# Kernel tuning notes

Measured on AMD Instinct MI355X. Metric: run time of the kernel, lower is better.

## Reference

```python
import jax, jax.numpy as jnp
import numpy as np

N_HEADS = 32
N_KV = 16
HEAD_DIM = 128
REPEATS = N_HEADS // N_KV
ROPE_THETA = 10000.0
SOFTCAP = 50.0
SCALE = 1.0 / np.sqrt(144.0)


def _rope_cos_sin(L, dtype):
    half = HEAD_DIM // 2
    inv_freq = 1.0 / (ROPE_THETA ** (jnp.arange(0, HEAD_DIM, 2, dtype=jnp.float32) / HEAD_DIM))
    ang = jnp.arange(L, dtype=jnp.float32)[:, None] * inv_freq[None, :]  # [L, half]
    return jnp.cos(ang).astype(dtype), jnp.sin(ang).astype(dtype)


def _apply_rope(t, cos, sin):
    # t: [B, H, L, D]; non-traditional (rotate-half) RoPE
    half = HEAD_DIM // 2
    t1, t2 = t[..., :half], t[..., half:]
    c = cos[None, None, :, :]
    s = sin[None, None, :, :]
    return jnp.concatenate([t1 * c - t2 * s, t2 * c + t1 * s], axis=-1)


def setup_inputs() -> dict:
    key = jax.random.key(0)
    k1, k2, k3, k4, k5 = jax.random.split(key, 5)
    B, L, D = 1, 2048, 4608
    x = jax.random.normal(k1, (B, L, D), dtype=jnp.float32)
    wq = jax.random.normal(k2, (N_HEADS * HEAD_DIM, D), dtype=jnp.float32) * 0.02
    wk = jax.random.normal(k3, (N_KV * HEAD_DIM, D), dtype=jnp.float32) * 0.02
    wv = jax.random.normal(k4, (N_KV * HEAD_DIM, D), dtype=jnp.float32) * 0.02
    wo = jax.random.normal(k5, (D, N_HEADS * HEAD_DIM), dtype=jnp.float32) * 0.02
    mask = jnp.tril(jnp.ones((L, L), dtype=bool))  # causal
    return {"x": x, "mask": mask, "wq": wq, "wk": wk, "wv": wv, "wo": wo}


def reference(x, mask, wq, wk, wv, wo):
    B, L, D = x.shape
    q = (x @ wq.T).reshape(B, L, N_HEADS, HEAD_DIM).transpose(0, 2, 1, 3)
    k = (x @ wk.T).reshape(B, L, N_KV, HEAD_DIM).transpose(0, 2, 1, 3)
    v = (x @ wv.T).reshape(B, L, N_KV, HEAD_DIM).transpose(0, 2, 1, 3)

    cos, sin = _rope_cos_sin(L, x.dtype)
    q = _apply_rope(q, cos, sin) * jnp.asarray(SCALE, x.dtype)
    k = _apply_rope(k, cos, sin)

    # GQA: group queries per kv head -> [B, n_kv, repeats, L, D]
    qg = q.reshape(B, N_KV, REPEATS, L, HEAD_DIM)
    scores = jnp.einsum("bgrqd,bgkd->bgrqk", qg, k)
    scores = jnp.tanh(scores / SOFTCAP) * SOFTCAP
    neg = jnp.asarray(jnp.finfo(scores.dtype).min, scores.dtype)
    scores = jnp.where(mask[None, None, None, :, :], scores, neg)
    probs = jax.nn.softmax(scores, axis=-1)
    out = jnp.einsum("bgrqk,bgkd->bgrqd", probs, v)  # [B, n_kv, rep, L, D]
    out = out.reshape(B, N_HEADS, L, HEAD_DIM).transpose(0, 2, 1, 3).reshape(B, L, -1)
    return out @ wo.T
```

## Files before the change

### kernel.cpp

```cpp
#include <hip/hip_runtime.h>
#include <hip/hip_bf16.h>
#include <math.h>

typedef unsigned short u16;
typedef __attribute__((ext_vector_type(8))) short s16x8;
typedef __attribute__((ext_vector_type(4))) float f32x4;

#define SCALE 0.083333333333333329f
#define LDO 4128

__device__ __forceinline__ u16 f2bf(float f) {
    unsigned u = __float_as_uint(f);
    unsigned r = 0x7fffu + ((u >> 16) & 1u);
    return (u16)((u + r) >> 16);
}
__device__ __forceinline__ float bf2f(u16 v) {
    return __uint_as_float(((unsigned)v) << 16);
}

__global__ __launch_bounds__(256) void cast_kernel(const float* __restrict__ in,
                                                   u16* __restrict__ out) {
    size_t i = ((size_t)blockIdx.x * 256 + threadIdx.x) * 4;
    float4 v = *(const float4*)(in + i);
    ushort4 o;
    o.x = f2bf(v.x); o.y = f2bf(v.y); o.z = f2bf(v.z); o.w = f2bf(v.w);
    *(ushort4*)(out + i) = o;
}

__global__ __launch_bounds__(256) void cast_pad_kernel(const float* __restrict__ in,
                                                       u16* __restrict__ out) {
    size_t i = ((size_t)blockIdx.x * 256 + threadIdx.x) * 4;
    size_t row = i >> 12;
    int col = (int)(i & 4095);
    float4 v = *(const float4*)(in + i);
    ushort4 o;
    o.x = f2bf(v.x); o.y = f2bf(v.y); o.z = f2bf(v.z); o.w = f2bf(v.w);
    *(ushort4*)(out + row * LDO + col) = o;
}

__global__ __launch_bounds__(256) void rope_table_kernel(float* __restrict__ cosT,
                                                         float* __restrict__ sinT) {
    int idx = blockIdx.x * 256 + threadIdx.x;
    int i = idx & 63, pos = idx >> 6;
    float inv = __expf(-((float)i / 64.0f) * 9.210340371976184f);
    float ang = (float)pos * inv;
    cosT[idx] = cosf(ang);
    sinT[idx] = sinf(ang);
}

__global__ __launch_bounds__(256) void rope_q_kernel(const u16* __restrict__ T16,
                                                     u16* __restrict__ Qb,
                                                     const float* __restrict__ cosT,
                                                     const float* __restrict__ sinT) {
    int idx = blockIdx.x * 256 + threadIdx.x;
    int i = idx & 63;
    int head = (idx >> 6) & 31;
    int pos = idx >> 11;
    size_t rbase = (size_t)pos * 8192 + head * 128 + i;
    float t1 = bf2f(T16[rbase]), t2 = bf2f(T16[rbase + 64]);
    float c = cosT[(pos << 6) + i], s = sinT[(pos << 6) + i];
    size_t wbase = (size_t)pos * 4096 + head * 128 + i;
    Qb[wbase]      = f2bf((t1 * c - t2 * s) * SCALE);
    Qb[wbase + 64] = f2bf((t2 * c + t1 * s) * SCALE);
}

__global__ __launch_bounds__(256) void rope_k_kernel(const u16* __restrict__ T16,
                                                     u16* __restrict__ Kb,
                                                     const float* __restrict__ cosT,
                                                     const float* __restrict__ sinT) {
    int idx = blockIdx.x * 256 + threadIdx.x;
    int i = idx & 63;
    int head = (idx >> 6) & 15;
    int pos = idx >> 10;
    size_t rbase = (size_t)pos * 8192 + 4096 + head * 128 + i;
    float t1 = bf2f(T16[rbase]), t2 = bf2f(T16[rbase + 64]);
    float c = cosT[(pos << 6) + i], s = sinT[(pos << 6) + i];
    size_t wbase = (size_t)pos * 2048 + head * 128 + i;
    Kb[wbase]      = f2bf(t1 * c - t2 * s);
    Kb[wbase + 64] = f2bf(t2 * c + t1 * s);
}

__global__ __launch_bounds__(256) void vtrans_kernel(const u16* __restrict__ T16,
                                                     u16* __restrict__ Vt) {
    __shared__ u16 tile[32][33];
    int bc = (blockIdx.x & 63) << 5;
    int bl = (blockIdx.x >> 6) << 5;
    int x = threadIdx.x & 31, y = threadIdx.x >> 5;
    #pragma unroll
    for (int yy = y; yy < 32; yy += 8)
        tile[yy][x] = T16[(size_t)(bl + yy) * 8192 + 6144 + bc + x];
    __syncthreads();
    #pragma unroll
    for (int yy = y; yy < 32; yy += 8)
        Vt[(size_t)(bc + yy) * 2048 + bl + x] = tile[x][yy];
}

#define STAGE_A(buf, ktt, l)                                                            \
    __builtin_amdgcn_global_load_lds(                                                   \
        (const __attribute__((address_space(1))) unsigned int*)(aSrc + (size_t)(ktt) * 64 + (size_t)(l) * 64 * lda), \
        (__attribute__((address_space(3))) unsigned int*)(&lds[buf][0][(l) * 4096 + ldsoff]), 16, 0, 0)
#define STAGE_B(buf, ktt, l)                                                            \
    __builtin_amdgcn_global_load_lds(                                                   \
        (const __attribute__((address_space(1))) unsigned int*)(bSrc + (size_t)(ktt) * 64 + (size_t)(l) * 64 * ldb), \
        (__attribute__((address_space(3))) unsigned int*)(&lds[buf][1][(l) * 4096 + ldsoff]), 16, 0, 0)

template<bool OUT_BF16>
__device__ __forceinline__ void gemm256_core(const u16* __restrict__ A,
                                             const u16* __restrict__ B,
                                             void* __restrict__ C,
                                             int N, int K, int lda, int ldb,
                                             int bm, int bn,
                                             u16 (&lds)[2][2][16384]) {
    int t = threadIdx.x;
    int lane = t & 63, wave = t >> 6;
    int wm = wave >> 2, wn = wave & 3;
    int fr = lane & 15, fq = lane >> 4;
    int sw = (fr & 7) << 4;

    int srow = wave * 8 + (lane >> 3);
    int scb = ((lane & 7) * 16) ^ (((lane >> 3) & 7) << 4);
    const u16* aSrc = A + (size_t)(bm * 256 + srow) * lda + (scb >> 1);
    const u16* bSrc = B + (size_t)(bn * 256 + srow) * ldb + (scb >> 1);
    int ldsoff = wave * 512;

    f32x4 acc[8][4];
    #pragma unroll
    for (int m = 0; m < 8; m++)
        #pragma unroll
        for (int n = 0; n < 4; n++)
            acc[m][n] = (f32x4){0.f, 0.f, 0.f, 0.f};

    STAGE_B(0, 0, 0); STAGE_B(0, 0, 1); STAGE_B(0, 0, 2); STAGE_B(0, 0, 3);
    STAGE_A(0, 0, 0); STAGE_A(0, 0, 1); STAGE_A(0, 0, 2); STAGE_A(0, 0, 3);

    int nt = K >> 6;
    for (int it = 0; it < nt; ++it) {
        int cur = it & 1, nxt = cur ^ 1;
        bool more = (it + 1 < nt);
        const char* Ab = (const char*)&lds[cur][0][0];
        const char* Bb = (const char*)&lds[cur][1][0];
        int cb0 = (fq * 16) ^ sw;
        int cb1 = (64 + fq * 16) ^ sw;

        if (more) {
            STAGE_B(nxt, it + 1, 0); STAGE_B(nxt, it + 1, 1);
            __builtin_amdgcn_sched_barrier(0);
            asm volatile("s_waitcnt vmcnt(2)" ::: "memory");
        } else {
            asm volatile("s_waitcnt vmcnt(0)" ::: "memory");
        }
        __builtin_amdgcn_s_barrier();
        s16x8 b0[4], a0[4];
        #pragma unroll
        for (int n = 0; n < 4; ++n)
            b0[n] = *(const s16x8*)(Bb + (wn * 64 + n * 16 + fr) * 128 + cb0);
        #pragma unroll
        for (int m = 0; m < 4; ++m)
            a0[m] = *(const s16x8*)(Ab + (wm * 128 + m * 16 + fr) * 128 + cb0);
        __builtin_amdgcn_s_setprio(1);
        #pragma unroll
        for (int m = 0; m < 4; ++m)
            #pragma unroll
            for (int n = 0; n < 4; ++n)
                acc[m][n] = __builtin_amdgcn_mfma_f32_16x16x32_bf16(a0[m], b0[n], acc[m][n], 0, 0, 0);
        __builtin_amdgcn_s_setprio(0);
        s16x8 a1[4];
        #pragma unroll
        for (int m = 0; m < 4; ++m)
            a1[m] = *(const s16x8*)(Ab + (wm * 128 + (4 + m) * 16 + fr) * 128 + cb0);
        __builtin_amdgcn_s_barrier();

        if (more) { STAGE_B(nxt, it + 1, 2); STAGE_B(nxt, it + 1, 3); }
        __builtin_amdgcn_s_setprio(1);
        #pragma unroll
        for (int m = 0; m < 4; ++m)
            #pragma unroll
            for (int n = 0; n < 4; ++n)
                acc[4 + m][n] = __builtin_amdgcn_mfma_f32_16x16x32_bf16(a1[m], b0[n], acc[4 + m][n], 0, 0, 0);
        __builtin_amdgcn_s_setprio(0);
        s16x8 b1[4], a2[4];
        #pragma unroll
        for (int n = 0; n < 4; ++n)
            b1[n] = *(const s16x8*)(Bb + (wn * 64 + n * 16 + fr) * 128 + cb1);
        #pragma unroll
        for (int m = 0; m < 4; ++m)
            a2[m] = *(const s16x8*)(Ab + (wm * 128 + m * 16 + fr) * 128 + cb1);
        __builtin_amdgcn_s_barrier();

        if (more) {
            STAGE_A(nxt, it + 1, 0); STAGE_A(nxt, it + 1, 1);
            STAGE_A(nxt, it + 1, 2); STAGE_A(nxt, it + 1, 3);
        }
        __builtin_amdgcn_s_setprio(1);
        #pragma unroll
        for (int m = 0; m < 4; ++m)
            #pragma unroll
            for (int n = 0; n < 4; ++n)
                acc[m][n] = __builtin_amdgcn_mfma_f32_16x16x32_bf16(a2[m], b1[n], acc[m][n], 0, 0, 0);
        __builtin_amdgcn_s_setprio(0);
        s16x8 a3[4];
        #pragma unroll
        for (int m = 0; m < 4; ++m)
            a3[m] = *(const s16x8*)(Ab + (wm * 128 + (4 + m) * 16 + fr) * 128 + cb1);
        __builtin_amdgcn_s_barrier();

        __builtin_amdgcn_s_setprio(1);
        #pragma unroll
        for (int m = 0; m < 4; ++m)
            #pragma unroll
            for (int n = 0; n < 4; ++n)
                acc[4 + m][n] = __builtin_amdgcn_mfma_f32_16x16x32_bf16(a3[m], b1[n], acc[4 + m][n], 0, 0, 0);
        __builtin_amdgcn_s_setprio(0);
        __builtin_amdgcn_s_barrier();
    }

    #pragma unroll
    for (int m = 0; m < 8; ++m) {
        int row = bm * 256 + wm * 128 + m * 16 + fq * 4;
        #pragma unroll
        for (int n = 0; n < 4; ++n) {
            int col = bn * 256 + wn * 64 + n * 16 + fr;
            #pragma unroll
            for (int r = 0; r < 4; ++r) {
                if (OUT_BF16) ((u16*)C)[(size_t)(row + r) * N + col] = f2bf(acc[m][n][r]);
                else          ((float*)C)[(size_t)(row + r) * N + col] = acc[m][n][r];
            }
        }
    }
}

__global__ __launch_bounds__(512) void gemm256_qkv(const u16* __restrict__ A,
                                                   const u16* __restrict__ B,
                                                   u16* __restrict__ C, int K) {
    __shared__ u16 lds[2][2][16384];
    int bid = blockIdx.x;
    int x = bid & 7, j = bid >> 3;
    int bn = x * 4 + (j & 3);
    int bm = j >> 2;
    gemm256_core<true>(A, B, C, 8192, K, K, K, bm, bn, lds);
}

__global__ __launch_bounds__(512) void gemm256_out(const u16* __restrict__ A,
                                                   const u16* __restrict__ B,
                                                   float* __restrict__ C, int K) {
    __shared__ u16 lds[2][2][16384];
    int bid = blockIdx.x;
    int j = (bid & 7) * 18 + (bid >> 3);
    int bm = j & 7;
    int bn = j >> 3;
    gemm256_core<false>(A, B, C, 4608, K, LDO, LDO, bm, bn, lds);
}

__global__ __launch_bounds__(256) void attn_kernel(const u16* __restrict__ Qb,
                                                   const u16* __restrict__ Kb,
                                                   const u16* __restrict__ Vt,
                                                   u16* __restrict__ Ob) {
    __shared__ u16 Ks[64 * 128];
    __shared__ u16 Vs[128 * 64];
    __shared__ u16 Pst[4 * 1024];

    int bid = blockIdx.x;
    int hq = bid & 31;
    int qb = 31 - (bid >> 5);
    int g = hq >> 1;
    int t = threadIdx.x;
    int lane = t & 63, wave = t >> 6;
    int fr = lane & 15, fq = lane >> 4;
    int sw = (fr & 7) << 4;
    int qrow0 = qb * 64 + wave * 16;
    u16* Pw = &Pst[wave * 1024];

    s16x8 qf[4];
    #pragma unroll
    for (int s = 0; s < 4; s++)
        qf[s] = *(const s16x8*)&Qb[(size_t)(qrow0 + fr) * 4096 + hq * 128 + s * 32 + fq * 8];

    f32x4 o[8];
    #pragma unroll
    for (int c = 0; c < 8; c++) o[c] = (f32x4){0.f, 0.f, 0.f, 0.f};
    float liacc[4] = {0.f, 0.f, 0.f, 0.f};

    int w4 = wave * 4;
    int nT = qb + 1;
    for (int kt = 0; kt < nT; kt++) {
        int kv0 = kt << 6;
        __syncthreads();
        #pragma unroll
        for (int i = 0; i < 4; i++) {
            int li_ = w4 + i;
            int rk = li_ * 4 + (lane >> 4);
            int cbk = ((lane & 15) * 16) ^ ((rk & 7) << 4);
            const u16* srcK = Kb + (size_t)(kv0 + rk) * 2048 + g * 128 + (cbk >> 1);
            __builtin_amdgcn_global_load_lds(
                (const __attribute__((address_space(1))) unsigned int*)srcK,
                (__attribute__((address_space(3))) unsigned int*)(Ks + li_ * 512), 16, 0, 0);
            int rv = li_ * 8 + (lane >> 3);
            int cbv = ((lane & 7) * 16) ^ ((rv & 7) << 4);
            const u16* srcV = Vt + (size_t)(g * 128 + rv) * 2048 + kv0 + (cbv >> 1);
            __builtin_amdgcn_global_load_lds(
                (const __attribute__((address_space(1))) unsigned int*)srcV,
                (__attribute__((address_space(3))) unsigned int*)(Vs + li_ * 512), 16, 0, 0);
        }
        __syncthreads();

        if (kv0 <= qrow0 + 15) {
            f32x4 sf[4];
            #pragma unroll
            for (int j = 0; j < 4; j++) sf[j] = (f32x4){0.f, 0.f, 0.f, 0.f};
            #pragma unroll
            for (int j = 0; j < 4; j++)
                #pragma unroll
                for (int s = 0; s < 4; s++) {
                    s16x8 kf = *(const s16x8*)&Ks[(j * 16 + fr) * 128 + (((s * 64 + fq * 16) ^ sw) >> 1)];
                    sf[j] = __builtin_amdgcn_mfma_f32_16x16x32_bf16(qf[s], kf, sf[j], 0, 0, 0);
                }
            #pragma unroll
            for (int j = 0; j < 4; j++)
                #pragma unroll
                for (int r = 0; r < 4; r++) {
                    float s_ = sf[j][r];
                    float e = __builtin_amdgcn_exp2f(s_ * 0.05770780163f);
                    float p = __builtin_amdgcn_exp2f(-144.2695041f * __builtin_amdgcn_rcpf(e + 1.0f));
                    int colk = kv0 + j * 16 + fr;
                    int rowq = qrow0 + fq * 4 + r;
                    p = (colk > rowq) ? 0.0f : p;
                    sf[j][r] = p;
                    liacc[r] += p;
                }
            #pragma unroll
            for (int j = 0; j < 4; j++)
                #pragma unroll
                for (int r = 0; r < 4; r++) {
                    int row = fq * 4 + r, col = j * 16 + fr;
                    int byteoff = (row * 128 + col * 2) ^ ((row & 7) << 4);
                    *(u16*)((char*)Pw + byteoff) = f2bf(sf[j][r]);
                }
            #pragma unroll
            for (int s = 0; s < 2; s++) {
                int rbyte = (fr * 128 + s * 64 + fq * 16) ^ sw;
                s16x8 pf = *(const s16x8*)((const char*)Pw + rbyte);
                #pragma unroll
                for (int c = 0; c < 8; c++) {
                    s16x8 vf = *(const s16x8*)&Vs[(c * 16 + fr) * 64 + (((s * 64 + fq * 16) ^ sw) >> 1)];
                    o[c] = __builtin_amdgcn_mfma_f32_16x16x32_bf16(pf, vf, o[c], 0, 0, 0);
                }
            }
        }
    }
    #pragma unroll
    for (int d = 1; d < 16; d <<= 1)
        #pragma unroll
        for (int r = 0; r < 4; r++)
            liacc[r] += __shfl_xor(liacc[r], d);
    float rli[4];
    #pragma unroll
    for (int r = 0; r < 4; r++) rli[r] = __builtin_amdgcn_rcpf(liacc[r]);
    #pragma unroll
    for (int c = 0; c < 8; c++)
        #pragma unroll
        for (int r = 0; r < 4; r++) {
            int rowq = qrow0 + fq * 4 + r;
            Ob[(size_t)rowq * LDO + hq * 128 + c * 16 + fr] = f2bf(o[c][r] * rli[r]);
        }
}

extern "C" void kernel_launch(void* const* d_in, const int* in_sizes, int n_in,
                              void* d_out, int out_size, void* d_ws, size_t ws_size,
                              hipStream_t stream) {
    const float* x  = (const float*)d_in[0];
    const float* wq = (const float*)d_in[2];
    const float* wk = (const float*)d_in[3];
    const float* wv = (const float*)d_in[4];
    const float* wo = (const float*)d_in[5];
    float* out = (float*)d_out;

    char* w = (char*)d_ws;
    u16*   xb   = (u16*)(w);
    u16*   wb   = (u16*)(w + 18874368);
    u16*   T16  = (u16*)(w + 94371840);
    u16*   Ob   = (u16*)(w + 127926272);
    u16*   Qbuf = (u16*)(w + 144834560);
    u16*   Kbuf = (u16*)(w + 161611776);
    u16*   Vt   = (u16*)(w + 170000384);
    float* cosT = (float*)(w + 178388992);
    float* sinT = (float*)(w + 178913280);

    rope_table_kernel<<<512, 256, 0, stream>>>(cosT, sinT);
    cast_kernel<<<9216, 256, 0, stream>>>(x, xb);

    cast_kernel<<<18432, 256, 0, stream>>>(wq, wb);
    cast_kernel<<<9216, 256, 0, stream>>>(wk, wb + (size_t)4096 * 4608);
    cast_kernel<<<9216, 256, 0, stream>>>(wv, wb + (size_t)6144 * 4608);

    gemm256_qkv<<<256, 512, 0, stream>>>(xb, wb, T16, 4608);

    rope_q_kernel<<<16384, 256, 0, stream>>>(T16, Qbuf, cosT, sinT);
    rope_k_kernel<<<8192, 256, 0, stream>>>(T16, Kbuf, cosT, sinT);
    vtrans_kernel<<<4096, 256, 0, stream>>>(T16, Vt);

    attn_kernel<<<1024, 256, 0, stream>>>(Qbuf, Kbuf, Vt, Ob);

    cast_pad_kernel<<<18432, 256, 0, stream>>>(wo, wb);
    gemm256_out<<<144, 512, 0, stream>>>(Ob, wb, out, 4096);
}
```

Measured before the change: 398.7 us.

## Fuse fp32-to-bf16 weight conversion into GEMM B-tile staging

```diff
diff --git a/kernel.cpp b/kernel.cpp
--- a/kernel.cpp
+++ b/kernel.cpp
@@ -4,6 +4,7 @@
 
 typedef unsigned short u16;
 typedef __attribute__((ext_vector_type(8))) short s16x8;
+typedef __attribute__((ext_vector_type(8))) unsigned short u16x8;
 typedef __attribute__((ext_vector_type(4))) float f32x4;
 
 #define SCALE 0.083333333333333329f
@@ -25,17 +26,6 @@
     ushort4 o;
     o.x = f2bf(v.x); o.y = f2bf(v.y); o.z = f2bf(v.z); o.w = f2bf(v.w);
     *(ushort4*)(out + i) = o;
-}
-
-__global__ __launch_bounds__(256) void cast_pad_kernel(const float* __restrict__ in,
-                                                       u16* __restrict__ out) {
-    size_t i = ((size_t)blockIdx.x * 256 + threadIdx.x) * 4;
-    size_t row = i >> 12;
-    int col = (int)(i & 4095);
-    float4 v = *(const float4*)(in + i);
-    ushort4 o;
-    o.x = f2bf(v.x); o.y = f2bf(v.y); o.z = f2bf(v.z); o.w = f2bf(v.w);
-    *(ushort4*)(out + row * LDO + col) = o;
 }
 
 __global__ __launch_bounds__(256) void rope_table_kernel(float* __restrict__ cosT,
@@ -99,16 +89,112 @@
     __builtin_amdgcn_global_load_lds(                                                   \
         (const __attribute__((address_space(1))) unsigned int*)(aSrc + (size_t)(ktt) * 64 + (size_t)(l) * 64 * lda), \
         (__attribute__((address_space(3))) unsigned int*)(&lds[buf][0][(l) * 4096 + ldsoff]), 16, 0, 0)
-#define STAGE_B(buf, ktt, l)                                                            \
-    __builtin_amdgcn_global_load_lds(                                                   \
-        (const __attribute__((address_space(1))) unsigned int*)(bSrc + (size_t)(ktt) * 64 + (size_t)(l) * 64 * ldb), \
-        (__attribute__((address_space(3))) unsigned int*)(&lds[buf][1][(l) * 4096 + ldsoff]), 16, 0, 0)
+
+#define LOADB(REG, KTT)                                                                 \
+    _Pragma("unroll")                                                                   \
+    for (int l = 0; l < 4; ++l) {                                                       \
+        const float* p = bSrcF + (size_t)l * 64 * ldbf + (size_t)(KTT) * 64;            \
+        REG[l][0] = *(const float4*)p;                                                  \
+        REG[l][1] = *(const float4*)(p + 4);                                            \
+    }
+
+#define CVTW(REG, BUF)                                                                  \
+    _Pragma("unroll")                                                                   \
+    for (int l = 0; l < 4; ++l) {                                                       \
+        u16x8 pk;                                                                       \
+        pk[0] = f2bf(REG[l][0].x); pk[1] = f2bf(REG[l][0].y);                           \
+        pk[2] = f2bf(REG[l][0].z); pk[3] = f2bf(REG[l][0].w);                           \
+        pk[4] = f2bf(REG[l][1].x); pk[5] = f2bf(REG[l][1].y);                           \
+        pk[6] = f2bf(REG[l][1].z); pk[7] = f2bf(REG[l][1].w);                           \
+        *(u16x8*)((char*)&lds[BUF][1][0] + l * 8192 + bwb) = pk;                        \
+    }
+
+#define GTILE(CUR, NXT, RL, RW, T)                                                      \
+  {                                                                                     \
+    bool ld2 = ((T) + 2 < nt);                                                          \
+    bool stA = ((T) + 1 < nt);                                                          \
+    if (ld2) {                                                                          \
+        LOADB(RL, (T) + 2);                                                             \
+        __builtin_amdgcn_sched_barrier(0);                                              \
+        asm volatile("s_waitcnt vmcnt(8)" ::: "memory");                                \
+    } else {                                                                            \
+        asm volatile("s_waitcnt vmcnt(0)" ::: "memory");                                \
+    }                                                                                   \
+    __builtin_amdgcn_s_barrier();                                                       \
+    const char* Ab = (const char*)&lds[CUR][0][0];                                      \
+    const char* Bb = (const char*)&lds[CUR][1][0];                                      \
+    int cb0 = (fq * 16) ^ sw;                                                           \
+    int cb1 = (64 + fq * 16) ^ sw;                                                      \
+                                                                           \
+    if (stA) { STAGE_A(NXT, (T) + 1, 0); STAGE_A(NXT, (T) + 1, 1); }                    \
+    s16x8 b0[4], a0[4];                                                                 \
+    _Pragma("unroll")                                                                   \
+    for (int n = 0; n < 4; ++n)                                                         \
+        b0[n] = *(const s16x8*)(Bb + (wn * 64 + n * 16 + fr) * 128 + cb0);              \
+    _Pragma("unroll")                                                                   \
+    for (int m = 0; m < 4; ++m)                                                         \
+        a0[m] = *(const s16x8*)(Ab + (wm * 128 + m * 16 + fr) * 128 + cb0);             \
+    __builtin_amdgcn_s_setprio(1);                                                      \
+    _Pragma("unroll")                                                                   \
+    for (int m = 0; m < 4; ++m)                                                         \
+        _Pragma("unroll")                                                               \
+        for (int n = 0; n < 4; ++n)                                                     \
+            acc[m][n] = __builtin_amdgcn_mfma_f32_16x16x32_bf16(a0[m], b0[n], acc[m][n], 0, 0, 0); \
+    __builtin_amdgcn_s_setprio(0);                                                      \
+    s16x8 a1[4];                                                                        \
+    _Pragma("unroll")                                                                   \
+    for (int m = 0; m < 4; ++m)                                                         \
+        a1[m] = *(const s16x8*)(Ab + (wm * 128 + (4 + m) * 16 + fr) * 128 + cb0);       \
+    __builtin_amdgcn_s_barrier();                                                       \
+                                                                           \
+    if (stA) { STAGE_A(NXT, (T) + 1, 2); STAGE_A(NXT, (T) + 1, 3); }                    \
+    __builtin_amdgcn_s_setprio(1);                                                      \
+    _Pragma("unroll")                                                                   \
+    for (int m = 0; m < 4; ++m)                                                         \
+        _Pragma("unroll")                                                               \
+        for (int n = 0; n < 4; ++n)                                                     \
+            acc[4 + m][n] = __builtin_amdgcn_mfma_f32_16x16x32_bf16(a1[m], b0[n], acc[4 + m][n], 0, 0, 0); \
+    __builtin_amdgcn_s_setprio(0);                                                      \
+    s16x8 b1[4], a2[4];                                                                 \
+    _Pragma("unroll")                                                                   \
+    for (int n = 0; n < 4; ++n)                                                         \
+        b1[n] = *(const s16x8*)(Bb + (wn * 64 + n * 16 + fr) * 128 + cb1);              \
+    _Pragma("unroll")                                                                   \
+    for (int m = 0; m < 4; ++m)                                                         \
+        a2[m] = *(const s16x8*)(Ab + (wm * 128 + m * 16 + fr) * 128 + cb1);             \
+    __builtin_amdgcn_s_barrier();                                                       \
+                                                                           \
+    __builtin_amdgcn_s_setprio(1);                                                      \
+    _Pragma("unroll")                                                                   \
+    for (int m = 0; m < 4; ++m)                                                         \
+        _Pragma("unroll")                                                               \
+        for (int n = 0; n < 4; ++n)                                                     \
+            acc[m][n] = __builtin_amdgcn_mfma_f32_16x16x32_bf16(a2[m], b1[n], acc[m][n], 0, 0, 0); \
+    __builtin_amdgcn_s_setprio(0);                                                      \
+    s16x8 a3[4];                                                                        \
+    _Pragma("unroll")                                                                   \
+    for (int m = 0; m < 4; ++m)                                                         \
+        a3[m] = *(const s16x8*)(Ab + (wm * 128 + (4 + m) * 16 + fr) * 128 + cb1);       \
+    __builtin_amdgcn_s_barrier();                                                       \
+                                \
+    if (stA) { CVTW(RW, NXT); }                                                         \
+    __builtin_amdgcn_s_setprio(1);                                                      \
+    _Pragma("unroll")                                                                   \
+    for (int m = 0; m < 4; ++m)                                                         \
+        _Pragma("unroll")                                                               \
+        for (int n = 0; n < 4; ++n)                                                     \
+            acc[4 + m][n] = __builtin_amdgcn_mfma_f32_16x16x32_bf16(a3[m], b1[n], acc[4 + m][n], 0, 0, 0); \
+    __builtin_amdgcn_s_setprio(0);                                                      \
+    asm volatile("s_waitcnt lgkmcnt(0)" ::: "memory");                                  \
+    __builtin_amdgcn_sched_barrier(0);                                                  \
+    __builtin_amdgcn_s_barrier();                                                       \
+  }
 
 template<bool OUT_BF16>
 __device__ __forceinline__ void gemm256_core(const u16* __restrict__ A,
-                                             const u16* __restrict__ B,
+                                             const float* __restrict__ Bpanel,
                                              void* __restrict__ C,
-                                             int N, int K, int lda, int ldb,
+                                             int N, int K, int lda, int ldbf,
                                              int bm, int bn,
                                              u16 (&lds)[2][2][16384]) {
     int t = threadIdx.x;
@@ -120,8 +206,11 @@
     int srow = wave * 8 + (lane >> 3);
     int scb = ((lane & 7) * 16) ^ (((lane >> 3) & 7) << 4);
     const u16* aSrc = A + (size_t)(bm * 256 + srow) * lda + (scb >> 1);
-    const u16* bSrc = B + (size_t)(bn * 256 + srow) * ldb + (scb >> 1);
     int ldsoff = wave * 512;
+
+    int brow = wave * 8 + (lane >> 3);
+    const float* bSrcF = Bpanel + (size_t)brow * ldbf + (lane & 7) * 8;
+    int bwb = brow * 128 + (((lane & 7) * 16) ^ ((brow & 7) << 4));
 
     f32x4 acc[8][4];
     #pragma unroll
@@ -130,88 +219,21 @@
         for (int n = 0; n < 4; n++)
             acc[m][n] = (f32x4){0.f, 0.f, 0.f, 0.f};
 
-    STAGE_B(0, 0, 0); STAGE_B(0, 0, 1); STAGE_B(0, 0, 2); STAGE_B(0, 0, 3);
+    float4 rE[4][2], rO[4][2];
+    int nt = K >> 6;
+
+    LOADB(rE, 0);
+    LOADB(rO, 1);
     STAGE_A(0, 0, 0); STAGE_A(0, 0, 1); STAGE_A(0, 0, 2); STAGE_A(0, 0, 3);
-
-    int nt = K >> 6;
-    for (int it = 0; it < nt; ++it) {
-        int cur = it & 1, nxt = cur ^ 1;
-        bool more = (it + 1 < nt);
-        const char* Ab = (const char*)&lds[cur][0][0];
-        const char* Bb = (const char*)&lds[cur][1][0];
-        int cb0 = (fq * 16) ^ sw;
-        int cb1 = (64 + fq * 16) ^ sw;
-
-        if (more) {
-            STAGE_B(nxt, it + 1, 0); STAGE_B(nxt, it + 1, 1);
-            __builtin_amdgcn_sched_barrier(0);
-            asm volatile("s_waitcnt vmcnt(2)" ::: "memory");
-        } else {
-            asm volatile("s_waitcnt vmcnt(0)" ::: "memory");
-        }
-        __builtin_amdgcn_s_barrier();
-        s16x8 b0[4], a0[4];
-        #pragma unroll
-        for (int n = 0; n < 4; ++n)
-            b0[n] = *(const s16x8*)(Bb + (wn * 64 + n * 16 + fr) * 128 + cb0);
-        #pragma unroll
-        for (int m = 0; m < 4; ++m)
-            a0[m] = *(const s16x8*)(Ab + (wm * 128 + m * 16 + fr) * 128 + cb0);
-        __builtin_amdgcn_s_setprio(1);
-        #pragma unroll
-        for (int m = 0; m < 4; ++m)
-            #pragma unroll
-            for (int n = 0; n < 4; ++n)
-                acc[m][n] = __builtin_amdgcn_mfma_f32_16x16x32_bf16(a0[m], b0[n], acc[m][n], 0, 0, 0);
-        __builtin_amdgcn_s_setprio(0);
-        s16x8 a1[4];
-        #pragma unroll
-        for (int m = 0; m < 4; ++m)
-            a1[m] = *(const s16x8*)(Ab + (wm * 128 + (4 + m) * 16 + fr) * 128 + cb0);
-        __builtin_amdgcn_s_barrier();
-
-        if (more) { STAGE_B(nxt, it + 1, 2); STAGE_B(nxt, it + 1, 3); }
-        __builtin_amdgcn_s_setprio(1);
-        #pragma unroll
-        for (int m = 0; m < 4; ++m)
-            #pragma unroll
-            for (int n = 0; n < 4; ++n)
-                acc[4 + m][n] = __builtin_amdgcn_mfma_f32_16x16x32_bf16(a1[m], b0[n], acc[4 + m][n], 0, 0, 0);
-        __builtin_amdgcn_s_setprio(0);
-        s16x8 b1[4], a2[4];
-        #pragma unroll
-        for (int n = 0; n < 4; ++n)
-            b1[n] = *(const s16x8*)(Bb + (wn * 64 + n * 16 + fr) * 128 + cb1);
-        #pragma unroll
-        for (int m = 0; m < 4; ++m)
-            a2[m] = *(const s16x8*)(Ab + (wm * 128 + m * 16 + fr) * 128 + cb1);
-        __builtin_amdgcn_s_barrier();
-
-        if (more) {
-            STAGE_A(nxt, it + 1, 0); STAGE_A(nxt, it + 1, 1);
-            STAGE_A(nxt, it + 1, 2); STAGE_A(nxt, it + 1, 3);
-        }
-        __builtin_amdgcn_s_setprio(1);
-        #pragma unroll
-        for (int m = 0; m < 4; ++m)
-            #pragma unroll
-            for (int n = 0; n < 4; ++n)
-                acc[m][n] = __builtin_amdgcn_mfma_f32_16x16x32_bf16(a2[m], b1[n], acc[m][n], 0, 0, 0);
-        __builtin_amdgcn_s_setprio(0);
-        s16x8 a3[4];
-        #pragma unroll
-        for (int m = 0; m < 4; ++m)
-            a3[m] = *(const s16x8*)(Ab + (wm * 128 + (4 + m) * 16 + fr) * 128 + cb1);
-        __builtin_amdgcn_s_barrier();
-
-        __builtin_amdgcn_s_setprio(1);
-        #pragma unroll
-        for (int m = 0; m < 4; ++m)
-            #pragma unroll
-            for (int n = 0; n < 4; ++n)
-                acc[4 + m][n] = __builtin_amdgcn_mfma_f32_16x16x32_bf16(a3[m], b1[n], acc[4 + m][n], 0, 0, 0);
-        __builtin_amdgcn_s_setprio(0);
-        __builtin_amdgcn_s_barrier();
+    __builtin_amdgcn_sched_barrier(0);
+    asm volatile("s_waitcnt vmcnt(12)" ::: "memory");
+    CVTW(rE, 0);
+    asm volatile("s_waitcnt lgkmcnt(0)" ::: "memory");
+    __builtin_amdgcn_sched_barrier(0);
+
+    for (int it = 0; it < nt; it += 2) {
+        GTILE(0, 1, rE, rO, it);
+        GTILE(1, 0, rO, rE, it + 1);
     }
 
     #pragma unroll
@@ -230,25 +252,31 @@
 }
 
 __global__ __launch_bounds__(512) void gemm256_qkv(const u16* __restrict__ A,
-                                                   const u16* __restrict__ B,
+                                                   const float* __restrict__ wq,
+                                                   const float* __restrict__ wk,
+                                                   const float* __restrict__ wv,
                                                    u16* __restrict__ C, int K) {
     __shared__ u16 lds[2][2][16384];
     int bid = blockIdx.x;
     int x = bid & 7, j = bid >> 3;
     int bn = x * 4 + (j & 3);
     int bm = j >> 2;
-    gemm256_core<true>(A, B, C, 8192, K, K, K, bm, bn, lds);
+    const float* Bp;
+    if (bn < 16)      Bp = wq + (size_t)bn * 256 * K;
+    else if (bn < 24) Bp = wk + (size_t)(bn - 16) * 256 * K;
+    else              Bp = wv + (size_t)(bn - 24) * 256 * K;
+    gemm256_core<true>(A, Bp, C, 8192, K, K, K, bm, bn, lds);
 }
 
 __global__ __launch_bounds__(512) void gemm256_out(const u16* __restrict__ A,
-                                                   const u16* __restrict__ B,
+                                                   const float* __restrict__ wo,
                                                    float* __restrict__ C, int K) {
     __shared__ u16 lds[2][2][16384];
     int bid = blockIdx.x;
     int j = (bid & 7) * 18 + (bid >> 3);
     int bm = j & 7;
     int bn = j >> 3;
-    gemm256_core<false>(A, B, C, 4608, K, LDO, LDO, bm, bn, lds);
+    gemm256_core<false>(A, wo + (size_t)bn * 256 * K, C, 4608, K, LDO, K, bm, bn, lds);
 }
 
 __global__ __launch_bounds__(256) void attn_kernel(const u16* __restrict__ Qb,
@@ -376,23 +404,18 @@
 
     char* w = (char*)d_ws;
     u16*   xb   = (u16*)(w);
-    u16*   wb   = (u16*)(w + 18874368);
-    u16*   T16  = (u16*)(w + 94371840);
-    u16*   Ob   = (u16*)(w + 127926272);
-    u16*   Qbuf = (u16*)(w + 144834560);
-    u16*   Kbuf = (u16*)(w + 161611776);
-    u16*   Vt   = (u16*)(w + 170000384);
-    float* cosT = (float*)(w + 178388992);
-    float* sinT = (float*)(w + 178913280);
+    u16*   T16  = (u16*)(w + 18874368);
+    u16*   Ob   = (u16*)(w + 52428800);
+    u16*   Qbuf = (u16*)(w + 69337088);
+    u16*   Kbuf = (u16*)(w + 86114304);
+    u16*   Vt   = (u16*)(w + 94502912);
+    float* cosT = (float*)(w + 102891520);
+    float* sinT = (float*)(w + 103415808);
 
     rope_table_kernel<<<512, 256, 0, stream>>>(cosT, sinT);
     cast_kernel<<<9216, 256, 0, stream>>>(x, xb);
 
-    cast_kernel<<<18432, 256, 0, stream>>>(wq, wb);
-    cast_kernel<<<9216, 256, 0, stream>>>(wk, wb + (size_t)4096 * 4608);
-    cast_kernel<<<9216, 256, 0, stream>>>(wv, wb + (size_t)6144 * 4608);
-
-    gemm256_qkv<<<256, 512, 0, stream>>>(xb, wb, T16, 4608);
+    gemm256_qkv<<<256, 512, 0, stream>>>(xb, wq, wk, wv, T16, 4608);
 
     rope_q_kernel<<<16384, 256, 0, stream>>>(T16, Qbuf, cosT, sinT);
     rope_k_kernel<<<8192, 256, 0, stream>>>(T16, Kbuf, cosT, sinT);
@@ -400,6 +423,5 @@
 
     attn_kernel<<<1024, 256, 0, stream>>>(Qbuf, Kbuf, Vt, Ob);
 
-    cast_pad_kernel<<<18432, 256, 0, stream>>>(wo, wb);
-    gemm256_out<<<144, 512, 0, stream>>>(Ob, wb, out, 4096);
-}
+    gemm256_out<<<144, 512, 0, stream>>>(Ob, wo, out, 4096);
+}
```

New measurement: 1.116 ms. 180% more time.
